# Kernel tuning notes

Measured on AMD Instinct MI355X. Metric: run time of the kernel, lower is better.

The kernel has to match this reference:

```python
import jax, jax.numpy as jnp
import numpy as np

N_NODES = 4096
DEG_HALF = 16
MAX_E = 64
D = 128
H = 4
L = 2
N_SPECIES = 4
R_CUT = 5.0
R_TRANS = 3.0


def _layer_norm(x, w, b, eps=1e-5):
    m = jnp.mean(x, axis=-1, keepdims=True)
    v = jnp.mean((x - m) ** 2, axis=-1, keepdims=True)
    return (x - m) * jax.lax.rsqrt(v + eps) * w + b


def _transformer(x, radial_mask, p):
    # x: (N, MAX_E, D); radial_mask: (N, MAX_E). Pre-LN transformer whose
    # attention weights are reweighted by the radial cutoff mask over keys.
    ln1_w, ln1_b, qkv_w, qkv_b, out_w, out_b, ln2_w, ln2_b, m1_w, m1_b, m2_w, m2_b = p
    n, s, d = x.shape
    dh = d // H
    scale = np.float32(1.0 / np.sqrt(dh))
    for l in range(L):
        h = _layer_norm(x, ln1_w[l], ln1_b[l])
        qkv = h @ qkv_w[l] + qkv_b[l]  # (n, s, 3d)
        q, k, v = jnp.split(qkv, 3, axis=-1)
        q = q.reshape(n, s, H, dh).transpose(0, 2, 1, 3)
        k = k.reshape(n, s, H, dh).transpose(0, 2, 1, 3)
        v = v.reshape(n, s, H, dh).transpose(0, 2, 1, 3)
        a = jax.nn.softmax(jnp.einsum("nhqc,nhkc->nhqk", q, k) * scale, axis=-1)
        a = a * radial_mask[:, None, None, :]
        a = a / (jnp.sum(a, axis=-1, keepdims=True) + 1e-9)
        o = jnp.einsum("nhqk,nhkc->nhqc", a, v).transpose(0, 2, 1, 3).reshape(n, s, d)
        x = x + o @ out_w[l] + out_b[l]
        h = _layer_norm(x, ln2_w[l], ln2_b[l])
        x = x + jax.nn.gelu(h @ m1_w[l] + m1_b[l]) @ m2_w[l] + m2_b[l]
    return x


def _forward(edge_vectors, enc_cart_w, enc_center_emb, enc_neighbor_emb, enc_comp_w,
             t0, t1, gnn_w, last_w, comp_w,
             species_index, centers, neighbors, nef_indices, nef_mask,
             nef_to_edges_neighbor, corresponding_edges):
    r = jnp.sqrt(jnp.sum(edge_vectors ** 2, axis=-1))
    radial = jnp.where(r < R_TRANS, 1.0,
                       0.5 * (jnp.cos(jnp.pi * (r - R_TRANS) / (R_CUT - R_TRANS)) + 1.0))
    radial = jnp.where(r < R_CUT, radial, 0.0)
    eic = species_index[centers]
    ein = species_index[neighbors]
    # edge_array_to_nef gathers
    ev_nef = edge_vectors[nef_indices]                  # (N, MAX_E, 3)
    rm = jnp.where(nef_mask, radial[nef_indices], 0.0)  # (N, MAX_E)
    enc = jnp.concatenate([ev_nef @ enc_cart_w,
                           enc_center_emb[eic[nef_indices]],
                           enc_neighbor_emb[ein[nef_indices]]], axis=-1)
    feat = enc @ enc_comp_w                             # (N, MAX_E, D)
    feat = _transformer(feat, rm, t0)
    # one message-passing round (num_gnn_layers=2 -> 1 MP layer)
    edge_feat = feat[centers, nef_to_edges_neighbor]    # NEF -> edge list, (E, D)
    new = jnp.concatenate([edge_feat, edge_feat[corresponding_edges]], axis=-1) @ gnn_w
    new = _transformer(new[nef_indices], rm, t1)        # edge list -> NEF
    feat = feat + new
    node_features = jnp.sum(feat * rm[..., None], axis=1)  # masked scatter-sum
    return node_features @ last_w + comp_w[species_index][:, None]  # (N, 1)


def setup_inputs() -> dict:
    rng = np.random.default_rng(0)
    src = np.repeat(np.arange(N_NODES), DEG_HALF)
    dst = (src + rng.integers(1, N_NODES, size=src.shape[0])) % N_NODES
    centers = np.concatenate([src, dst]).astype(np.int64)
    neighbors = np.concatenate([dst, src]).astype(np.int64)
    E = centers.shape[0]
    corresponding_edges = np.concatenate([np.arange(E // 2, E), np.arange(E // 2)]).astype(np.int64)
    order = np.argsort(centers, kind="stable")
    sc = centers[order]
    starts = np.searchsorted(sc, np.arange(N_NODES))
    ranks = np.arange(E) - starts[sc]
    assert ranks.max() < MAX_E
    nef_indices = np.zeros((N_NODES, MAX_E), np.int64)
    nef_mask = np.zeros((N_NODES, MAX_E), bool)
    nef_indices[sc, ranks] = order
    nef_mask[sc, ranks] = True
    nef_to_edges_neighbor = np.zeros(E, np.int64)
    nef_to_edges_neighbor[order] = ranks
    half = rng.standard_normal((E // 2, 3)) * 1.6
    edge_vectors = np.concatenate([half, -half]).astype(np.float32)
    species_index = rng.integers(0, N_SPECIES, N_NODES).astype(np.int64)

    keys = iter(jax.random.split(jax.random.key(0), 80))

    def lin(shape, fan_in):
        return jax.random.normal(next(keys), shape, jnp.float32) / np.float32(np.sqrt(fan_in))

    inp = {
        "edge_vectors": jnp.asarray(edge_vectors),
        "enc_cart_w": lin((3, D), 3),
        "enc_center_emb": lin((N_SPECIES, D), 1),
        "enc_neighbor_emb": lin((N_SPECIES, D), 1),
        "enc_comp_w": lin((3 * D, D), 3 * D),
        "gnn_w": lin((2 * D, D), 2 * D),
        "last_w": lin((D, 1), D),
        "comp_w": lin((N_SPECIES,), 1),
        "species_index": jnp.asarray(species_index),
        "centers": jnp.asarray(centers),
        "neighbors": jnp.asarray(neighbors),
        "nef_indices": jnp.asarray(nef_indices),
        "nef_mask": jnp.asarray(nef_mask),
        "nef_to_edges_neighbor": jnp.asarray(nef_to_edges_neighbor),
        "corresponding_edges": jnp.asarray(corresponding_edges),
    }
    for t in ("t0", "t1"):
        inp[t + "_ln1_w"] = jnp.ones((L, D), jnp.float32)
        inp[t + "_ln1_b"] = jnp.zeros((L, D), jnp.float32)
        inp[t + "_qkv_w"] = lin((L, D, 3 * D), D)
        inp[t + "_qkv_b"] = jnp.zeros((L, 3 * D), jnp.float32)
        inp[t + "_out_w"] = lin((L, D, D), D)
        inp[t + "_out_b"] = jnp.zeros((L, D), jnp.float32)
        inp[t + "_ln2_w"] = jnp.ones((L, D), jnp.float32)
        inp[t + "_ln2_b"] = jnp.zeros((L, D), jnp.float32)
        inp[t + "_mlp1_w"] = lin((L, D, 4 * D), D)
        inp[t + "_mlp1_b"] = jnp.zeros((L, 4 * D), jnp.float32)
        inp[t + "_mlp2_w"] = lin((L, 4 * D, D), 4 * D)
        inp[t + "_mlp2_b"] = jnp.zeros((L, D), jnp.float32)
    return inp


def reference(edge_vectors, enc_cart_w, enc_center_emb, enc_neighbor_emb, enc_comp_w,
              t0_ln1_w, t0_ln1_b, t0_qkv_w, t0_qkv_b, t0_out_w, t0_out_b,
              t0_ln2_w, t0_ln2_b, t0_mlp1_w, t0_mlp1_b, t0_mlp2_w, t0_mlp2_b,
              t1_ln1_w, t1_ln1_b, t1_qkv_w, t1_qkv_b, t1_out_w, t1_out_b,
              t1_ln2_w, t1_ln2_b, t1_mlp1_w, t1_mlp1_b, t1_mlp2_w, t1_mlp2_b,
              gnn_w, last_w, comp_w,
              species_index, centers, neighbors, nef_indices, nef_mask,
              nef_to_edges_neighbor, corresponding_edges):
    t0 = (t0_ln1_w, t0_ln1_b, t0_qkv_w, t0_qkv_b, t0_out_w, t0_out_b,
          t0_ln2_w, t0_ln2_b, t0_mlp1_w, t0_mlp1_b, t0_mlp2_w, t0_mlp2_b)
    t1 = (t1_ln1_w, t1_ln1_b, t1_qkv_w, t1_qkv_b, t1_out_w, t1_out_b,
          t1_ln2_w, t1_ln2_b, t1_mlp1_w, t1_mlp1_b, t1_mlp2_w, t1_mlp2_b)
    return _forward(edge_vectors, enc_cart_w, enc_center_emb, enc_neighbor_emb, enc_comp_w,
                    t0, t1, gnn_w, last_w, comp_w,
                    species_index, centers, neighbors, nef_indices, nef_mask,
                    nef_to_edges_neighbor, corresponding_edges)
```

## Files before the change

kernel.cpp:

```cpp
#include <hip/hip_runtime.h>

typedef short s8v __attribute__((ext_vector_type(8)));
typedef float f4v __attribute__((ext_vector_type(4)));

#define MFMA16(a,b,c) __builtin_amdgcn_mfma_f32_16x16x32_bf16((a),(b),(c),0,0,0)

#define N_NODES 4096
#define N_EDGE  131072
#define ATT_SCALE 0.17677669529663687f
#define GELU_C   0.7978845608028654f

__device__ __forceinline__ unsigned short f2bf(float f) {
  union { float f; unsigned u; } v; v.f = f;
  return (unsigned short)((v.u + 0x8000u) >> 16);
}
__device__ __forceinline__ unsigned short f2bf_rne(float f) {
  union { float f; unsigned u; } v; v.f = f;
  unsigned r = v.u + 0x7fffu + ((v.u >> 16) & 1u);
  return (unsigned short)(r >> 16);
}
__device__ __forceinline__ float bf2f(short s) {
  union { unsigned u; float f; } v;
  v.u = ((unsigned)(unsigned short)s) << 16;
  return v.f;
}
__device__ __forceinline__ int iclamp(int v, int lo, int hi) {
  return v < lo ? lo : (v > hi ? hi : v);
}


__global__ void k_tr(const float* __restrict__ src, short* __restrict__ dst,
                     int L, int K, int N) {
  int idx = blockIdx.x * 256 + threadIdx.x;
  int tot = L * K * N;
  if (idx >= tot) return;
  int l = idx / (K * N);
  int r = idx - l * (K * N);
  int k = r / N;
  int n = r - k * N;
  dst[l * K * N + n * K + k] = (short)f2bf_rne(src[idx]);
}

__global__ void k_tabs(const float* __restrict__ cart, const float* __restrict__ cemb,
                       const float* __restrict__ nemb, const float* __restrict__ comp,
                       float* __restrict__ tabs) {
  int idx = blockIdx.x * 256 + threadIdx.x;
  if (idx >= 1408) return;
  float s = 0.f;
  if (idx < 384) {
    int i = idx >> 7, d = idx & 127;
    for (int j = 0; j < 128; ++j) s += cart[i * 128 + j] * comp[j * 128 + d];
  } else if (idx < 896) {
    int i2 = idx - 384; int sp = i2 >> 7, d = i2 & 127;
    for (int j = 0; j < 128; ++j) s += cemb[sp * 128 + j] * comp[(128 + j) * 128 + d];
  } else {
    int i2 = idx - 896; int sp = i2 >> 7, d = i2 & 127;
    for (int j = 0; j < 128; ++j) s += nemb[sp * 128 + j] * comp[(256 + j) * 128 + d];
  }
  tabs[idx] = s;
}

__global__ void k_rm(const float* __restrict__ ev, const int* __restrict__ centers,
                     const int* __restrict__ nef2, float* __restrict__ rm) {
  int e = blockIdx.x * 256 + threadIdx.x;
  if (e >= N_EDGE) return;
  float x = ev[e*3], y = ev[e*3+1], z = ev[e*3+2];
  float r = sqrtf(x*x + y*y + z*z);
  float rad;
  if (r < 3.0f)      rad = 1.0f;
  else if (r < 5.0f) rad = 0.5f * (cosf(3.14159265358979f * (r - 3.0f) * 0.5f) + 1.0f);
  else               rad = 0.0f;
  int c  = iclamp(centers[e], 0, N_NODES - 1);
  int rk = iclamp(nef2[e], 0, 63);
  rm[c * 64 + rk] = rad;
}

__global__ __launch_bounds__(256) void k_enc(
    const float* __restrict__ ev, const int* __restrict__ nef,
    const int* __restrict__ centers, const int* __restrict__ neighbors,
    const int* __restrict__ species, const float* __restrict__ tabs,
    short* __restrict__ feat) {
  int n = blockIdx.x, t = threadIdx.x, j = t >> 2, qq = t & 3;
  int e = iclamp(nef[n * 64 + j], 0, N_EDGE - 1);
  float e0 = ev[e*3], e1 = ev[e*3+1], e2 = ev[e*3+2];
  int nc = iclamp(centers[e],   0, N_NODES - 1);
  int nn = iclamp(neighbors[e], 0, N_NODES - 1);
  int sc = iclamp(species[nc], 0, 3), sn = iclamp(species[nn], 0, 3);
  const float* m0 = tabs + qq*32;
  const float* m1 = tabs + 128 + qq*32;
  const float* m2 = tabs + 256 + qq*32;
  const float* tc = tabs + 384 + sc*128 + qq*32;
  const float* tn = tabs + 896 + sn*128 + qq*32;
  short* o = feat + ((size_t)(n*64 + j))*128 + qq*32;
  #pragma unroll
  for (int i = 0; i < 32; i += 2) {
    float a = e0*m0[i]   + e1*m1[i]   + e2*m2[i]   + tc[i]   + tn[i];
    float b = e0*m0[i+1] + e1*m1[i+1] + e2*m2[i+1] + tc[i+1] + tn[i+1];
    *(unsigned*)(o + i) = (unsigned)f2bf_rne(a) | ((unsigned)f2bf_rne(b) << 16);
  }
}


__device__ __forceinline__ void ln_sub(float (&xr)[4][2][4],
                                       const float* __restrict__ gw, const float* __restrict__ gb,
                                       float* red, short* hb, int wid, int quad, int l4) {
  #pragma unroll
  for (int mt = 0; mt < 4; ++mt)
    #pragma unroll
    for (int reg = 0; reg < 4; ++reg) {
      float a = xr[mt][0][reg] + xr[mt][1][reg];
      float s = xr[mt][0][reg]*xr[mt][0][reg] + xr[mt][1][reg]*xr[mt][1][reg];
      #pragma unroll
      for (int m = 1; m < 16; m <<= 1) { a += __shfl_xor(a, m); s += __shfl_xor(s, m); }
      if (l4 == 0) {
        int r = mt*16 + quad*4 + reg;
        red[(wid*64 + r)*2]     = a;
        red[(wid*64 + r)*2 + 1] = s;
      }
    }
  __syncthreads();
  int tid = threadIdx.x;
  if (tid < 64) {
    float a = 0.f, s = 0.f;
    #pragma unroll
    for (int w = 0; w < 4; ++w) { a += red[(w*64 + tid)*2]; s += red[(w*64 + tid)*2 + 1]; }
    float mean = a * (1.f/128.f);
    float var  = s * (1.f/128.f) - mean*mean;
    red[tid*2]     = mean;
    red[tid*2 + 1] = rsqrtf(var + 1e-5f);
  }
  __syncthreads();
  float gv[2], bv[2];
  #pragma unroll
  for (int nt = 0; nt < 2; ++nt) { int c = wid*32 + nt*16 + l4; gv[nt] = gw[c]; bv[nt] = gb[c]; }
  #pragma unroll
  for (int mt = 0; mt < 4; ++mt)
    #pragma unroll
    for (int reg = 0; reg < 4; ++reg) {
      int r = mt*16 + quad*4 + reg;
      float mean = red[r*2], inv = red[r*2 + 1];
      #pragma unroll
      for (int nt = 0; nt < 2; ++nt) {
        float h = (xr[mt][nt][reg] - mean) * inv * gv[nt] + bv[nt];
        hb[r*136 + wid*32 + nt*16 + l4] = (short)f2bf(h);
      }
    }
  __syncthreads();
}

__global__ __launch_bounds__(256, 3) void k_tf(
    short* __restrict__ x, const float* __restrict__ rm,
    const float* __restrict__ lnw1, const float* __restrict__ lnb1,
    const short* __restrict__ qkvT, const float* __restrict__ qkvb,
    const short* __restrict__ outT, const float* __restrict__ outb,
    const float* __restrict__ lnw2, const float* __restrict__ lnb2,
    const short* __restrict__ m1T, const float* __restrict__ m1b,
    const short* __restrict__ m2T, const float* __restrict__ m2b) {
  __shared__ __align__(16) char smem[53248];
  short* hb  = (short*)smem;
  short* kb  = (short*)(smem + 17408);
  short* vtb = (short*)(smem + 34816);
  float* red = (float*)(smem + 34816);

  const int tid = threadIdx.x;
  const int wid = tid >> 6;
  const int lane = tid & 63;
  const int l4 = lane & 15;
  const int quad = lane >> 4;
  const int n = blockIdx.x;

  float rv[4];
  #pragma unroll
  for (int n2 = 0; n2 < 4; ++n2) rv[n2] = rm[n*64 + n2*16 + l4];

  short* xg = x + (size_t)n * 64 * 128;
  float xr[4][2][4];
  #pragma unroll
  for (int mt = 0; mt < 4; ++mt)
    #pragma unroll
    for (int nt = 0; nt < 2; ++nt)
      #pragma unroll
      for (int reg = 0; reg < 4; ++reg)
        xr[mt][nt][reg] = bf2f(xg[(mt*16 + quad*4 + reg)*128 + wid*32 + nt*16 + l4]);

  for (int l = 0; l < 2; ++l) {
    const float* g1    = lnw1 + l*128;   const float* bb1   = lnb1 + l*128;
    const short* qkvTl = qkvT + l*49152; const float* qkvbl = qkvb + l*384;
    const short* outTl = outT + l*16384; const float* outbl = outb + l*128;
    const float* g2    = lnw2 + l*128;   const float* bb2   = lnb2 + l*128;
    const short* m1Tl  = m1T + l*65536;  const float* m1bl  = m1b + l*512;
    const short* m2Tl  = m2T + l*65536;  const float* m2bl  = m2b + l*128;

    __syncthreads();

    ln_sub(xr, g1, bb1, red, hb, wid, quad, l4);

    {
      s8v af[4][4];
      #pragma unroll
      for (int mt = 0; mt < 4; ++mt)
        #pragma unroll
        for (int k0 = 0; k0 < 4; ++k0)
          af[mt][k0] = *(const s8v*)(hb + (mt*16 + l4)*136 + k0*32 + quad*8);
      __syncthreads();

      #pragma unroll 2
      for (int j = 0; j < 6; ++j) {
        int col = wid*96 + j*16 + l4;
        s8v bf[4];
        #pragma unroll
        for (int k0 = 0; k0 < 4; ++k0)
          bf[k0] = *(const s8v*)(qkvTl + col*128 + k0*32 + quad*8);
        float bias = qkvbl[col];
        f4v acc[4];
        #pragma unroll
        for (int mt = 0; mt < 4; ++mt) { f4v zz = {0.f,0.f,0.f,0.f}; acc[mt] = zz; }
        #pragma unroll
        for (int k0 = 0; k0 < 4; ++k0)
          #pragma unroll
          for (int mt = 0; mt < 4; ++mt)
            acc[mt] = MFMA16(af[mt][k0], bf[k0], acc[mt]);
        if (col < 128) {
          #pragma unroll
          for (int mt = 0; mt < 4; ++mt)
            #pragma unroll
            for (int reg = 0; reg < 4; ++reg)
              hb[(mt*16 + quad*4 + reg)*136 + col] = (short)f2bf((acc[mt][reg] + bias) * ATT_SCALE);
        } else if (col < 256) {
          int c = col - 128;
          #pragma unroll
          for (int mt = 0; mt < 4; ++mt)
            #pragma unroll
            for (int reg = 0; reg < 4; ++reg)
              kb[(mt*16 + quad*4 + reg)*136 + c] = (short)f2bf(acc[mt][reg] + bias);
        } else {
          int c = col - 256;
          #pragma unroll
          for (int mt = 0; mt < 4; ++mt)
            #pragma unroll
            for (int reg = 0; reg < 4; ++reg)
              vtb[c*72 + (mt*16 + quad*4 + reg)] = (short)f2bf(acc[mt][reg] + bias);
        }
      }
    }
    __syncthreads();

    {
      const int h = wid;
      s8v aq[4], bk[4];
      #pragma unroll
      for (int mt = 0; mt < 4; ++mt)
        aq[mt] = *(const s8v*)(hb + (mt*16 + l4)*136 + h*32 + quad*8);
      #pragma unroll
      for (int n2 = 0; n2 < 4; ++n2)
        bk[n2] = *(const s8v*)(kb + (n2*16 + l4)*136 + h*32 + quad*8);
      f4v S[4][4];
      #pragma unroll
      for (int mt = 0; mt < 4; ++mt)
        #pragma unroll
        for (int n2 = 0; n2 < 4; ++n2) {
          f4v zz = {0.f,0.f,0.f,0.f};
          S[mt][n2] = MFMA16(aq[mt], bk[n2], zz);
        }

      #pragma unroll
      for (int mt = 0; mt < 4; ++mt)
        #pragma unroll
        for (int reg = 0; reg < 4; ++reg) {
          float mx = fmaxf(fmaxf(S[mt][0][reg], S[mt][1][reg]),
                           fmaxf(S[mt][2][reg], S[mt][3][reg]));
          mx = fmaxf(mx, __shfl_xor(mx, 1));
          mx = fmaxf(mx, __shfl_xor(mx, 2));
          mx = fmaxf(mx, __shfl_xor(mx, 4));
          mx = fmaxf(mx, __shfl_xor(mx, 8));
          float E = 0.f, W = 0.f;
          #pragma unroll
          for (int n2 = 0; n2 < 4; ++n2) {
            float e = __expf(S[mt][n2][reg] - mx);
            E += e; W += e * rv[n2];
            S[mt][n2][reg] = e * rv[n2];
          }
          E += __shfl_xor(E, 1); E += __shfl_xor(E, 2);
          E += __shfl_xor(E, 4); E += __shfl_xor(E, 8);
          W += __shfl_xor(W, 1); W += __shfl_xor(W, 2);
          W += __shfl_xor(W, 4); W += __shfl_xor(W, 8);
          float inv = 1.f / (W + 1e-9f * E);
          #pragma unroll
          for (int n2 = 0; n2 < 4; ++n2) S[mt][n2][reg] *= inv;
        }

      f4v o[4][2];
      #pragma unroll
      for (int mt = 0; mt < 4; ++mt)
        #pragma unroll
        for (int nt = 0; nt < 2; ++nt) { f4v zz = {0.f,0.f,0.f,0.f}; o[mt][nt] = zz; }
      for (int c = 0; c < 2; ++c) {
        #pragma unroll
        for (int mt = 0; mt < 4; ++mt)
          #pragma unroll
          for (int n2 = 0; n2 < 2; ++n2)
            #pragma unroll
            for (int reg = 0; reg < 4; ++reg)
              kb[(mt*16 + quad*4 + reg)*136 + h*32 + n2*16 + l4] =
                  (short)f2bf(S[mt][2*c + n2][reg]);
        s8v ap[4];
        #pragma unroll
        for (int mt = 0; mt < 4; ++mt)
          ap[mt] = *(const s8v*)(kb + (mt*16 + l4)*136 + h*32 + quad*8);
        #pragma unroll
        for (int nt = 0; nt < 2; ++nt) {
          s8v bv = *(const s8v*)(vtb + (h*32 + nt*16 + l4)*72 + c*32 + quad*8);
          #pragma unroll
          for (int mt = 0; mt < 4; ++mt)
            o[mt][nt] = MFMA16(ap[mt], bv, o[mt][nt]);
        }
      }
      #pragma unroll
      for (int mt = 0; mt < 4; ++mt)
        #pragma unroll
        for (int nt = 0; nt < 2; ++nt)
          #pragma unroll
          for (int reg = 0; reg < 4; ++reg)
            hb[(mt*16 + quad*4 + reg)*136 + h*32 + nt*16 + l4] = (short)f2bf(o[mt][nt][reg]);
    }
    __syncthreads();

    {
      s8v ao[4][4];
      #pragma unroll
      for (int mt = 0; mt < 4; ++mt)
        #pragma unroll
        for (int k0 = 0; k0 < 4; ++k0)
          ao[mt][k0] = *(const s8v*)(hb + (mt*16 + l4)*136 + k0*32 + quad*8);
      #pragma unroll
      for (int nt = 0; nt < 2; ++nt) {
        int c = wid*32 + nt*16 + l4;
        s8v bo[4];
        #pragma unroll
        for (int k0 = 0; k0 < 4; ++k0)
          bo[k0] = *(const s8v*)(outTl + c*128 + k0*32 + quad*8);
        float bias = outbl[c];
        #pragma unroll
        for (int mt = 0; mt < 4; ++mt) {
          f4v a2 = {xr[mt][nt][0], xr[mt][nt][1], xr[mt][nt][2], xr[mt][nt][3]};
          #pragma unroll
          for (int k0 = 0; k0 < 4; ++k0)
            a2 = MFMA16(ao[mt][k0], bo[k0], a2);
          #pragma unroll
          for (int reg = 0; reg < 4; ++reg)
            xr[mt][nt][reg] = a2[reg] + bias;
        }
      }
    }

    ln_sub(xr, g2, bb2, red, hb, wid, quad, l4);

    {
      s8v afm[4][4];
      #pragma unroll
      for (int mt = 0; mt < 4; ++mt)
        #pragma unroll
        for (int k0 = 0; k0 < 4; ++k0)
          afm[mt][k0] = *(const s8v*)(hb + (mt*16 + l4)*136 + k0*32 + quad*8);

      for (int cc = 0; cc < 4; ++cc) {
        short* G = (cc & 1) ? vtb : kb;
        #pragma unroll
        for (int nt = 0; nt < 2; ++nt) {
          int jc = cc*128 + wid*32 + nt*16 + l4;
          s8v bm[4];
          #pragma unroll
          for (int k0 = 0; k0 < 4; ++k0)
            bm[k0] = *(const s8v*)(m1Tl + jc*128 + k0*32 + quad*8);
          float bias = m1bl[jc];
          #pragma unroll
          for (int mt = 0; mt < 4; ++mt) {
            f4v a2 = {0.f,0.f,0.f,0.f};
            #pragma unroll
            for (int k0 = 0; k0 < 4; ++k0)
              a2 = MFMA16(afm[mt][k0], bm[k0], a2);
            #pragma unroll
            for (int reg = 0; reg < 4; ++reg) {
              float v = a2[reg] + bias;
              float zz2 = GELU_C * (v + 0.044715f * v * v * v);
              float ee = __expf(2.f * zz2);
              float th = 1.f - 2.f / (ee + 1.f);
              float gl = 0.5f * v * (1.f + th);
              G[(mt*16 + quad*4 + reg)*136 + wid*32 + nt*16 + l4] = (short)f2bf(gl);
            }
          }
        }
        s8v b2f[2][4];
        #pragma unroll
        for (int nt = 0; nt < 2; ++nt) {
          int c = wid*32 + nt*16 + l4;
          #pragma unroll
          for (int k0 = 0; k0 < 4; ++k0)
            b2f[nt][k0] = *(const s8v*)(m2Tl + c*512 + cc*128 + k0*32 + quad*8);
        }
        __syncthreads();
        s8v at4[4][4];
        #pragma unroll
        for (int mt = 0; mt < 4; ++mt)
          #pragma unroll
          for (int k0 = 0; k0 < 4; ++k0)
            at4[mt][k0] = *(const s8v*)(G + (mt*16 + l4)*136 + k0*32 + quad*8);
        #pragma unroll
        for (int nt = 0; nt < 2; ++nt) {
          #pragma unroll
          for (int mt = 0; mt < 4; ++mt) {
            f4v a2 = {xr[mt][nt][0], xr[mt][nt][1], xr[mt][nt][2], xr[mt][nt][3]};
            #pragma unroll
            for (int k0 = 0; k0 < 4; ++k0)
              a2 = MFMA16(at4[mt][k0], b2f[nt][k0], a2);
            #pragma unroll
            for (int reg = 0; reg < 4; ++reg)
              xr[mt][nt][reg] = a2[reg];
          }
        }
      }
      #pragma unroll
      for (int nt = 0; nt < 2; ++nt) {
        float b = m2bl[wid*32 + nt*16 + l4];
        #pragma unroll
        for (int mt = 0; mt < 4; ++mt)
          #pragma unroll
          for (int reg = 0; reg < 4; ++reg)
            xr[mt][nt][reg] += b;
      }
    }
  }

  #pragma unroll
  for (int mt = 0; mt < 4; ++mt)
    #pragma unroll
    for (int nt = 0; nt < 2; ++nt)
      #pragma unroll
      for (int reg = 0; reg < 4; ++reg)
        xg[(mt*16 + quad*4 + reg)*128 + wid*32 + nt*16 + l4] = (short)f2bf(xr[mt][nt][reg]);
}

__global__ __launch_bounds__(256) void k_gnn(
    const short* __restrict__ feat, const int* __restrict__ nef,
    const int* __restrict__ corr, const int* __restrict__ centers,
    const int* __restrict__ nef2, const short* __restrict__ gnnT,
    short* __restrict__ out) {
  __shared__ __align__(16) short Ab[64 * 264];
  int n = blockIdx.x, t = threadIdx.x;
  int wid = t >> 6, lane = t & 63, l4 = lane & 15, quad = lane >> 4;
  int j = t >> 2, qq = t & 3;
  int e  = iclamp(nef[n*64 + j], 0, N_EDGE - 1);
  int ce = iclamp(corr[e], 0, N_EDGE - 1);
  size_t r1 = ((size_t)iclamp(centers[e],  0, N_NODES-1) * 64 + iclamp(nef2[e],  0, 63)) * 128;
  size_t r2 = ((size_t)iclamp(centers[ce], 0, N_NODES-1) * 64 + iclamp(nef2[ce], 0, 63)) * 128;
  {
    const s8v* p1 = (const s8v*)(feat + r1 + qq*32);
    const s8v* p2 = (const s8v*)(feat + r2 + qq*32);
    #pragma unroll
    for (int ii = 0; ii < 4; ++ii) {
      *(s8v*)(Ab + j*264 + qq*32 + ii*8)       = p1[ii];
      *(s8v*)(Ab + j*264 + 128 + qq*32 + ii*8) = p2[ii];
    }
  }
  __syncthreads();
  f4v acc[4][2];
  #pragma unroll
  for (int mt = 0; mt < 4; ++mt)
    #pragma unroll
    for (int nt = 0; nt < 2; ++nt) { f4v zz = {0.f,0.f,0.f,0.f}; acc[mt][nt] = zz; }
  #pragma unroll
  for (int k0 = 0; k0 < 8; ++k0) {
    s8v a[4];
    #pragma unroll
    for (int mt = 0; mt < 4; ++mt)
      a[mt] = *(const s8v*)(Ab + (mt*16 + l4)*264 + k0*32 + quad*8);
    #pragma unroll
    for (int nt = 0; nt < 2; ++nt) {
      s8v b = *(const s8v*)(gnnT + (wid*32 + nt*16 + l4)*256 + k0*32 + quad*8);
      #pragma unroll
      for (int mt = 0; mt < 4; ++mt)
        acc[mt][nt] = MFMA16(a[mt], b, acc[mt][nt]);
    }
  }
  #pragma unroll
  for (int mt = 0; mt < 4; ++mt)
    #pragma unroll
    for (int nt = 0; nt < 2; ++nt)
      #pragma unroll
      for (int reg = 0; reg < 4; ++reg)
        out[((size_t)n*64 + mt*16 + quad*4 + reg)*128 + wid*32 + nt*16 + l4] =
            (short)f2bf(acc[mt][nt][reg]);
}

__global__ __launch_bounds__(256) void k_final(
    const short* __restrict__ feat, const short* __restrict__ buf2,
    const float* __restrict__ rm, const float* __restrict__ lastw,
    const float* __restrict__ compw, const int* __restrict__ species,
    float* __restrict__ out) {
  __shared__ float part[4];
  int n = blockIdx.x, t = threadIdx.x;
  int wid = t >> 6, lane = t & 63;
  int j = t >> 2, qq = t & 3;
  size_t base = ((size_t)n*64 + j)*128 + qq*32;
  float s = 0.f;
  #pragma unroll
  for (int i = 0; i < 32; ++i)
    s += (bf2f(feat[base + i]) + bf2f(buf2[base + i])) * lastw[qq*32 + i];
  s += __shfl_xor(s, 1);
  s += __shfl_xor(s, 2);
  float v = (qq == 0) ? s * rm[n*64 + j] : 0.f;
  v += __shfl_xor(v, 4);  v += __shfl_xor(v, 8);
  v += __shfl_xor(v, 16); v += __shfl_xor(v, 32);
  if (lane == 0) part[wid] = v;
  __syncthreads();
  if (t == 0) out[n] = part[0] + part[1] + part[2] + part[3]
                       + compw[iclamp(species[n], 0, 3)];
}


extern "C" void kernel_launch(void* const* d_in, const int* in_sizes, int n_in,
                              void* d_out, int out_size, void* d_ws, size_t ws_size,
                              hipStream_t stream) {
  const float* ev      = (const float*)d_in[0];
  const float* cart    = (const float*)d_in[1];
  const float* cemb    = (const float*)d_in[2];
  const float* nemb    = (const float*)d_in[3];
  const float* comp    = (const float*)d_in[4];
  const float* gnnw    = (const float*)d_in[5];
  const float* lastw   = (const float*)d_in[6];
  const float* compw   = (const float*)d_in[7];
  const int*   species = (const int*)d_in[8];
  const int*   centers = (const int*)d_in[9];
  const int*   neighbors = (const int*)d_in[10];
  const int*   nef     = (const int*)d_in[11];
  const int*   nef2    = (const int*)d_in[13];
  const int*   corr    = (const int*)d_in[14];

  const size_t OFF_RM   = 0;
  const size_t OFF_FEAT = 1048576;
  const size_t OFF_BUF2 = 68157440;
  const size_t OFF_TABS = 135266304;
  const size_t OFF_WBF  = 135271936;
  const size_t NEED     = 136910336;
  if (ws_size < NEED) return;

  char* ws = (char*)d_ws;
  float* rm   = (float*)(ws + OFF_RM);
  short* feat = (short*)(ws + OFF_FEAT);
  short* buf2 = (short*)(ws + OFF_BUF2);
  float* tabs = (float*)(ws + OFF_TABS);
  short* wbf  = (short*)(ws + OFF_WBF);

  short* t0q  = wbf + 0;
  short* t0o  = wbf + 98304;
  short* t0m1 = wbf + 131072;
  short* t0m2 = wbf + 262144;
  short* t1q  = wbf + 393216;
  short* t1o  = wbf + 491520;
  short* t1m1 = wbf + 524288;
  short* t1m2 = wbf + 655360;
  short* gnnT = wbf + 786432;

  hipMemsetAsync(rm, 0, 4096*64*sizeof(float), stream);

  k_tr<<<384, 256, 0, stream>>>((const float*)d_in[17], t0q,  2, 128, 384);
  k_tr<<<128, 256, 0, stream>>>((const float*)d_in[19], t0o,  2, 128, 128);
  k_tr<<<512, 256, 0, stream>>>((const float*)d_in[23], t0m1, 2, 128, 512);
  k_tr<<<512, 256, 0, stream>>>((const float*)d_in[25], t0m2, 2, 512, 128);
  k_tr<<<384, 256, 0, stream>>>((const float*)d_in[29], t1q,  2, 128, 384);
  k_tr<<<128, 256, 0, stream>>>((const float*)d_in[31], t1o,  2, 128, 128);
  k_tr<<<512, 256, 0, stream>>>((const float*)d_in[35], t1m1, 2, 128, 512);
  k_tr<<<512, 256, 0, stream>>>((const float*)d_in[37], t1m2, 2, 512, 128);
  k_tr<<<128, 256, 0, stream>>>(gnnw, gnnT, 1, 256, 128);
  k_tabs<<<6, 256, 0, stream>>>(cart, cemb, nemb, comp, tabs);
  k_rm<<<512, 256, 0, stream>>>(ev, centers, nef2, rm);
  k_enc<<<4096, 256, 0, stream>>>(ev, nef, centers, neighbors, species, tabs, feat);

  k_tf<<<4096, 256, 0, stream>>>(feat, rm,
      (const float*)d_in[15], (const float*)d_in[16], t0q, (const float*)d_in[18],
      t0o, (const float*)d_in[20], (const float*)d_in[21], (const float*)d_in[22],
      t0m1, (const float*)d_in[24], t0m2, (const float*)d_in[26]);

  k_gnn<<<4096, 256, 0, stream>>>(feat, nef, corr, centers, nef2, gnnT, buf2);

  k_tf<<<4096, 256, 0, stream>>>(buf2, rm,
      (const float*)d_in[27], (const float*)d_in[28], t1q, (const float*)d_in[30],
      t1o, (const float*)d_in[32], (const float*)d_in[33], (const float*)d_in[34],
      t1m1, (const float*)d_in[36], t1m2, (const float*)d_in[38]);

  k_final<<<4096, 256, 0, stream>>>(feat, buf2, rm, lastw, compw, species, (float*)d_out);
}
```

Measured before the change: 1.832 ms.

## Split transformer row tiles into halves to cut register pressure in k_tf

Restructures the k_tf transformer kernel to process the 64 rows as two 32-row halves in the QKV, attention, out-projection and MLP stages, so fewer A-fragments and accumulators are live at once. Biases are folded into the MFMA accumulator initial values, and GELU is rewritten as v*sigmoid form using a fast reciprocal. The softmax normalisation also uses the hardware rcp. The launch-bounds occupancy hint drops from 3 to 2, which trades occupancy for more registers per thread and may reduce latency hiding.

```diff
diff --git a/kernel.cpp b/kernel.cpp
--- a/kernel.cpp
+++ b/kernel.cpp
@@ -8,7 +8,7 @@
 #define N_NODES 4096
 #define N_EDGE  131072
 #define ATT_SCALE 0.17677669529663687f
-#define GELU_C   0.7978845608028654f
+#define NGC2     -1.5957691216057308f
 
 __device__ __forceinline__ unsigned short f2bf(float f) {
   union { float f; unsigned u; } v; v.f = f;
@@ -148,7 +148,7 @@
   __syncthreads();
 }
 
-__global__ __launch_bounds__(256, 3) void k_tf(
+__global__ __launch_bounds__(256, 2) void k_tf(
     short* __restrict__ x, const float* __restrict__ rm,
     const float* __restrict__ lnw1, const float* __restrict__ lnb1,
     const short* __restrict__ qkvT, const float* __restrict__ qkvb,
@@ -195,16 +195,15 @@
 
     ln_sub(xr, g1, bb1, red, hb, wid, quad, l4);
 
-    {
-      s8v af[4][4];
-      #pragma unroll
-      for (int mt = 0; mt < 4; ++mt)
+    for (int hh = 0; hh < 2; ++hh) {
+      s8v af[2][4];
+      #pragma unroll
+      for (int m2 = 0; m2 < 2; ++m2)
         #pragma unroll
         for (int k0 = 0; k0 < 4; ++k0)
-          af[mt][k0] = *(const s8v*)(hb + (mt*16 + l4)*136 + k0*32 + quad*8);
+          af[m2][k0] = *(const s8v*)(hb + ((hh*2 + m2)*16 + l4)*136 + k0*32 + quad*8);
       __syncthreads();
 
-      #pragma unroll 2
       for (int j = 0; j < 6; ++j) {
         int col = wid*96 + j*16 + l4;
         s8v bf[4];
@@ -212,34 +211,34 @@
         for (int k0 = 0; k0 < 4; ++k0)
           bf[k0] = *(const s8v*)(qkvTl + col*128 + k0*32 + quad*8);
         float bias = qkvbl[col];
-        f4v acc[4];
-        #pragma unroll
-        for (int mt = 0; mt < 4; ++mt) { f4v zz = {0.f,0.f,0.f,0.f}; acc[mt] = zz; }
+        f4v acc[2];
+        #pragma unroll
+        for (int m2 = 0; m2 < 2; ++m2) { f4v bb = {bias,bias,bias,bias}; acc[m2] = bb; }
         #pragma unroll
         for (int k0 = 0; k0 < 4; ++k0)
           #pragma unroll
-          for (int mt = 0; mt < 4; ++mt)
-            acc[mt] = MFMA16(af[mt][k0], bf[k0], acc[mt]);
+          for (int m2 = 0; m2 < 2; ++m2)
+            acc[m2] = MFMA16(af[m2][k0], bf[k0], acc[m2]);
         if (col < 128) {
           #pragma unroll
-          for (int mt = 0; mt < 4; ++mt)
+          for (int m2 = 0; m2 < 2; ++m2)
             #pragma unroll
             for (int reg = 0; reg < 4; ++reg)
-              hb[(mt*16 + quad*4 + reg)*136 + col] = (short)f2bf((acc[mt][reg] + bias) * ATT_SCALE);
+              hb[((hh*2+m2)*16 + quad*4 + reg)*136 + col] = (short)f2bf(acc[m2][reg] * ATT_SCALE);
         } else if (col < 256) {
           int c = col - 128;
           #pragma unroll
-          for (int mt = 0; mt < 4; ++mt)
+          for (int m2 = 0; m2 < 2; ++m2)
             #pragma unroll
             for (int reg = 0; reg < 4; ++reg)
-              kb[(mt*16 + quad*4 + reg)*136 + c] = (short)f2bf(acc[mt][reg] + bias);
+              kb[((hh*2+m2)*16 + quad*4 + reg)*136 + c] = (short)f2bf(acc[m2][reg]);
         } else {
           int c = col - 256;
           #pragma unroll
-          for (int mt = 0; mt < 4; ++mt)
+          for (int m2 = 0; m2 < 2; ++m2)
             #pragma unroll
             for (int reg = 0; reg < 4; ++reg)
-              vtb[c*72 + (mt*16 + quad*4 + reg)] = (short)f2bf(acc[mt][reg] + bias);
+              vtb[c*72 + (hh*2+m2)*16 + quad*4 + reg] = (short)f2bf(acc[m2][reg]);
         }
       }
     }
@@ -247,91 +246,96 @@
 
     {
       const int h = wid;
-      s8v aq[4], bk[4];
-      #pragma unroll
-      for (int mt = 0; mt < 4; ++mt)
-        aq[mt] = *(const s8v*)(hb + (mt*16 + l4)*136 + h*32 + quad*8);
+      s8v bk[4];
       #pragma unroll
       for (int n2 = 0; n2 < 4; ++n2)
         bk[n2] = *(const s8v*)(kb + (n2*16 + l4)*136 + h*32 + quad*8);
-      f4v S[4][4];
-      #pragma unroll
-      for (int mt = 0; mt < 4; ++mt)
-        #pragma unroll
-        for (int n2 = 0; n2 < 4; ++n2) {
-          f4v zz = {0.f,0.f,0.f,0.f};
-          S[mt][n2] = MFMA16(aq[mt], bk[n2], zz);
+
+      for (int hh = 0; hh < 2; ++hh) {
+        s8v aq[2];
+        #pragma unroll
+        for (int m2 = 0; m2 < 2; ++m2)
+          aq[m2] = *(const s8v*)(hb + ((hh*2+m2)*16 + l4)*136 + h*32 + quad*8);
+        f4v S[2][4];
+        #pragma unroll
+        for (int m2 = 0; m2 < 2; ++m2)
+          #pragma unroll
+          for (int n2 = 0; n2 < 4; ++n2) {
+            f4v zz = {0.f,0.f,0.f,0.f};
+            S[m2][n2] = MFMA16(aq[m2], bk[n2], zz);
+          }
+
+        #pragma unroll
+        for (int m2 = 0; m2 < 2; ++m2)
+          #pragma unroll
+          for (int reg = 0; reg < 4; ++reg) {
+            float mx = fmaxf(fmaxf(S[m2][0][reg], S[m2][1][reg]),
+                             fmaxf(S[m2][2][reg], S[m2][3][reg]));
+            mx = fmaxf(mx, __shfl_xor(mx, 1));
+            mx = fmaxf(mx, __shfl_xor(mx, 2));
+            mx = fmaxf(mx, __shfl_xor(mx, 4));
+            mx = fmaxf(mx, __shfl_xor(mx, 8));
+            float E = 0.f, W = 0.f;
+            #pragma unroll
+            for (int n2 = 0; n2 < 4; ++n2) {
+              float e = __expf(S[m2][n2][reg] - mx);
+              E += e; W += e * rv[n2];
+              S[m2][n2][reg] = e * rv[n2];
+            }
+            E += __shfl_xor(E, 1); E += __shfl_xor(E, 2);
+            E += __shfl_xor(E, 4); E += __shfl_xor(E, 8);
+            W += __shfl_xor(W, 1); W += __shfl_xor(W, 2);
+            W += __shfl_xor(W, 4); W += __shfl_xor(W, 8);
+            float inv = __builtin_amdgcn_rcpf(W + 1e-9f * E);
+            #pragma unroll
+            for (int n2 = 0; n2 < 4; ++n2) S[m2][n2][reg] *= inv;
+          }
+
+        f4v o[2][2];
+        #pragma unroll
+        for (int m2 = 0; m2 < 2; ++m2)
+          #pragma unroll
+          for (int nt = 0; nt < 2; ++nt) { f4v zz = {0.f,0.f,0.f,0.f}; o[m2][nt] = zz; }
+        for (int c = 0; c < 2; ++c) {
+          #pragma unroll
+          for (int m2 = 0; m2 < 2; ++m2)
+            #pragma unroll
+            for (int n2 = 0; n2 < 2; ++n2)
+              #pragma unroll
+              for (int reg = 0; reg < 4; ++reg)
+                kb[((hh*2+m2)*16 + quad*4 + reg)*136 + h*32 + n2*16 + l4] =
+                    (short)f2bf(S[m2][2*c + n2][reg]);
+          s8v ap[2];
+          #pragma unroll
+          for (int m2 = 0; m2 < 2; ++m2)
+            ap[m2] = *(const s8v*)(kb + ((hh*2+m2)*16 + l4)*136 + h*32 + quad*8);
+          #pragma unroll
+          for (int nt = 0; nt < 2; ++nt) {
+            s8v bv = *(const s8v*)(vtb + (h*32 + nt*16 + l4)*72 + c*32 + quad*8);
+            #pragma unroll
+            for (int m2 = 0; m2 < 2; ++m2)
+              o[m2][nt] = MFMA16(ap[m2], bv, o[m2][nt]);
+          }
         }
-
-      #pragma unroll
-      for (int mt = 0; mt < 4; ++mt)
-        #pragma unroll
-        for (int reg = 0; reg < 4; ++reg) {
-          float mx = fmaxf(fmaxf(S[mt][0][reg], S[mt][1][reg]),
-                           fmaxf(S[mt][2][reg], S[mt][3][reg]));
-          mx = fmaxf(mx, __shfl_xor(mx, 1));
-          mx = fmaxf(mx, __shfl_xor(mx, 2));
-          mx = fmaxf(mx, __shfl_xor(mx, 4));
-          mx = fmaxf(mx, __shfl_xor(mx, 8));
-          float E = 0.f, W = 0.f;
-          #pragma unroll
-          for (int n2 = 0; n2 < 4; ++n2) {
-            float e = __expf(S[mt][n2][reg] - mx);
-            E += e; W += e * rv[n2];
-            S[mt][n2][reg] = e * rv[n2];
-          }
-          E += __shfl_xor(E, 1); E += __shfl_xor(E, 2);
-          E += __shfl_xor(E, 4); E += __shfl_xor(E, 8);
-          W += __shfl_xor(W, 1); W += __shfl_xor(W, 2);
-          W += __shfl_xor(W, 4); W += __shfl_xor(W, 8);
-          float inv = 1.f / (W + 1e-9f * E);
-          #pragma unroll
-          for (int n2 = 0; n2 < 4; ++n2) S[mt][n2][reg] *= inv;
-        }
-
-      f4v o[4][2];
-      #pragma unroll
-      for (int mt = 0; mt < 4; ++mt)
-        #pragma unroll
-        for (int nt = 0; nt < 2; ++nt) { f4v zz = {0.f,0.f,0.f,0.f}; o[mt][nt] = zz; }
-      for (int c = 0; c < 2; ++c) {
-        #pragma unroll
-        for (int mt = 0; mt < 4; ++mt)
-          #pragma unroll
-          for (int n2 = 0; n2 < 2; ++n2)
+        #pragma unroll
+        for (int m2 = 0; m2 < 2; ++m2)
+          #pragma unroll
+          for (int nt = 0; nt < 2; ++nt)
             #pragma unroll
             for (int reg = 0; reg < 4; ++reg)
-              kb[(mt*16 + quad*4 + reg)*136 + h*32 + n2*16 + l4] =
-                  (short)f2bf(S[mt][2*c + n2][reg]);
-        s8v ap[4];
-        #pragma unroll
-        for (int mt = 0; mt < 4; ++mt)
-          ap[mt] = *(const s8v*)(kb + (mt*16 + l4)*136 + h*32 + quad*8);
-        #pragma unroll
-        for (int nt = 0; nt < 2; ++nt) {
-          s8v bv = *(const s8v*)(vtb + (h*32 + nt*16 + l4)*72 + c*32 + quad*8);
-          #pragma unroll
-          for (int mt = 0; mt < 4; ++mt)
-            o[mt][nt] = MFMA16(ap[mt], bv, o[mt][nt]);
-        }
-      }
-      #pragma unroll
-      for (int mt = 0; mt < 4; ++mt)
-        #pragma unroll
-        for (int nt = 0; nt < 2; ++nt)
-          #pragma unroll
-          for (int reg = 0; reg < 4; ++reg)
-            hb[(mt*16 + quad*4 + reg)*136 + h*32 + nt*16 + l4] = (short)f2bf(o[mt][nt][reg]);
+              hb[((hh*2+m2)*16 + quad*4 + reg)*136 + h*32 + nt*16 + l4] =
+                  (short)f2bf(o[m2][nt][reg]);
+      }
     }
     __syncthreads();
 
-    {
-      s8v ao[4][4];
-      #pragma unroll
-      for (int mt = 0; mt < 4; ++mt)
+    for (int hh = 0; hh < 2; ++hh) {
+      s8v ao[2][4];
+      #pragma unroll
+      for (int m2 = 0; m2 < 2; ++m2)
         #pragma unroll
         for (int k0 = 0; k0 < 4; ++k0)
-          ao[mt][k0] = *(const s8v*)(hb + (mt*16 + l4)*136 + k0*32 + quad*8);
+          ao[m2][k0] = *(const s8v*)(hb + ((hh*2+m2)*16 + l4)*136 + k0*32 + quad*8);
       #pragma unroll
       for (int nt = 0; nt < 2; ++nt) {
         int c = wid*32 + nt*16 + l4;
@@ -341,30 +345,31 @@
           bo[k0] = *(const s8v*)(outTl + c*128 + k0*32 + quad*8);
         float bias = outbl[c];
         #pragma unroll
-        for (int mt = 0; mt < 4; ++mt) {
-          f4v a2 = {xr[mt][nt][0], xr[mt][nt][1], xr[mt][nt][2], xr[mt][nt][3]};
+        for (int m2 = 0; m2 < 2; ++m2) {
+          int mt = hh*2 + m2;
+          f4v a2 = {xr[mt][nt][0] + bias, xr[mt][nt][1] + bias,
+                    xr[mt][nt][2] + bias, xr[mt][nt][3] + bias};
           #pragma unroll
           for (int k0 = 0; k0 < 4; ++k0)
-            a2 = MFMA16(ao[mt][k0], bo[k0], a2);
+            a2 = MFMA16(ao[m2][k0], bo[k0], a2);
           #pragma unroll
           for (int reg = 0; reg < 4; ++reg)
-            xr[mt][nt][reg] = a2[reg] + bias;
+            xr[mt][nt][reg] = a2[reg];
         }
       }
     }
 
     ln_sub(xr, g2, bb2, red, hb, wid, quad, l4);
 
-    {
-      s8v afm[4][4];
-      #pragma unroll
-      for (int mt = 0; mt < 4; ++mt)
-        #pragma unroll
-        for (int k0 = 0; k0 < 4; ++k0)
-          afm[mt][k0] = *(const s8v*)(hb + (mt*16 + l4)*136 + k0*32 + quad*8);
-
-      for (int cc = 0; cc < 4; ++cc) {
-        short* G = (cc & 1) ? vtb : kb;
+    for (int cc = 0; cc < 4; ++cc) {
+      short* G = (cc & 1) ? vtb : kb;
+      for (int hh = 0; hh < 2; ++hh) {
+        s8v afm[2][4];
+        #pragma unroll
+        for (int m2 = 0; m2 < 2; ++m2)
+          #pragma unroll
+          for (int k0 = 0; k0 < 4; ++k0)
+            afm[m2][k0] = *(const s8v*)(hb + ((hh*2+m2)*16 + l4)*136 + k0*32 + quad*8);
         #pragma unroll
         for (int nt = 0; nt < 2; ++nt) {
           int jc = cc*128 + wid*32 + nt*16 + l4;
@@ -374,60 +379,61 @@
             bm[k0] = *(const s8v*)(m1Tl + jc*128 + k0*32 + quad*8);
           float bias = m1bl[jc];
           #pragma unroll
-          for (int mt = 0; mt < 4; ++mt) {
-            f4v a2 = {0.f,0.f,0.f,0.f};
+          for (int m2 = 0; m2 < 2; ++m2) {
+            f4v a2 = {bias, bias, bias, bias};
             #pragma unroll
             for (int k0 = 0; k0 < 4; ++k0)
-              a2 = MFMA16(afm[mt][k0], bm[k0], a2);
+              a2 = MFMA16(afm[m2][k0], bm[k0], a2);
             #pragma unroll
             for (int reg = 0; reg < 4; ++reg) {
-              float v = a2[reg] + bias;
-              float zz2 = GELU_C * (v + 0.044715f * v * v * v);
-              float ee = __expf(2.f * zz2);
-              float th = 1.f - 2.f / (ee + 1.f);
-              float gl = 0.5f * v * (1.f + th);
-              G[(mt*16 + quad*4 + reg)*136 + wid*32 + nt*16 + l4] = (short)f2bf(gl);
+              float v = a2[reg];
+              float t = v * v;
+              float u = fmaf(0.044715f, t, 1.0f);
+              float w = v * u;
+              float e = __expf(NGC2 * w);
+              float gl = v * __builtin_amdgcn_rcpf(e + 1.0f);
+              G[((hh*2+m2)*16 + quad*4 + reg)*136 + wid*32 + nt*16 + l4] = (short)f2bf(gl);
             }
           }
         }
-        s8v b2f[2][4];
+      }
+      __syncthreads();
+      for (int hh = 0; hh < 2; ++hh) {
+        s8v at4[2][4];
+        #pragma unroll
+        for (int m2 = 0; m2 < 2; ++m2)
+          #pragma unroll
+          for (int k0 = 0; k0 < 4; ++k0)
+            at4[m2][k0] = *(const s8v*)(G + ((hh*2+m2)*16 + l4)*136 + k0*32 + quad*8);
         #pragma unroll
         for (int nt = 0; nt < 2; ++nt) {
           int c = wid*32 + nt*16 + l4;
+          s8v b2f[4];
           #pragma unroll
           for (int k0 = 0; k0 < 4; ++k0)
-            b2f[nt][k0] = *(const s8v*)(m2Tl + c*512 + cc*128 + k0*32 + quad*8);
-        }
-        __syncthreads();
-        s8v at4[4][4];
-        #pragma unroll
-        for (int mt = 0; mt < 4; ++mt)
-          #pragma unroll
-          for (int k0 = 0; k0 < 4; ++k0)
-            at4[mt][k0] = *(const s8v*)(G + (mt*16 + l4)*136 + k0*32 + quad*8);
-        #pragma unroll
-        for (int nt = 0; nt < 2; ++nt) {
-          #pragma unroll
-          for (int mt = 0; mt < 4; ++mt) {
+            b2f[k0] = *(const s8v*)(m2Tl + c*512 + cc*128 + k0*32 + quad*8);
+          #pragma unroll
+          for (int m2 = 0; m2 < 2; ++m2) {
+            int mt = hh*2 + m2;
             f4v a2 = {xr[mt][nt][0], xr[mt][nt][1], xr[mt][nt][2], xr[mt][nt][3]};
             #pragma unroll
             for (int k0 = 0; k0 < 4; ++k0)
-              a2 = MFMA16(at4[mt][k0], b2f[nt][k0], a2);
+              a2 = MFMA16(at4[m2][k0], b2f[k0], a2);
             #pragma unroll
             for (int reg = 0; reg < 4; ++reg)
               xr[mt][nt][reg] = a2[reg];
           }
         }
       }
-      #pragma unroll
-      for (int nt = 0; nt < 2; ++nt) {
-        float b = m2bl[wid*32 + nt*16 + l4];
-        #pragma unroll
-        for (int mt = 0; mt < 4; ++mt)
-          #pragma unroll
-          for (int reg = 0; reg < 4; ++reg)
-            xr[mt][nt][reg] += b;
-      }
+    }
+    #pragma unroll
+    for (int nt = 0; nt < 2; ++nt) {
+      float b = m2bl[wid*32 + nt*16 + l4];
+      #pragma unroll
+      for (int mt = 0; mt < 4; ++mt)
+        #pragma unroll
+        for (int reg = 0; reg < 4; ++reg)
+          xr[mt][nt][reg] += b;
     }
   }
 
```

Result: slower. 1.896 ms (+3.5%).
